# Kernel optimization log

Hardware: AMD Instinct MI355X
Metric: run time of the kernel (lower is better)

Reference implementation:

```python
import jax, jax.numpy as jnp
import numpy as np

N, DIM, H, D, S, B = 30000, 256, 8, 64, 32, 8
INNER = H * D


def setup_inputs() -> dict:
    key = jax.random.key(0)
    ks = jax.random.split(key, 16)
    def w(k, shape, fan_in):
        return jax.random.normal(k, shape, dtype=jnp.float32) / np.sqrt(fan_in)
    x = jax.random.normal(ks[0], (N, DIM), dtype=jnp.float32)
    batch = jnp.sort(jax.random.randint(ks[1], (N,), 0, B))
    return {
        'x': x,
        'batch': batch,
        'W_fx': w(ks[2], (DIM, INNER), DIM), 'b_fx': jnp.zeros((INNER,), jnp.float32),
        'W_x': w(ks[3], (DIM, INNER), DIM), 'b_x': jnp.zeros((INNER,), jnp.float32),
        'W_slice': w(ks[4], (D, S), D), 'b_slice': jnp.zeros((S,), jnp.float32),
        'graph_temp': 0.5 * jnp.ones((1, H, 1), jnp.float32),
        'W_q': w(ks[5], (D, D), D), 'W_k': w(ks[6], (D, D), D), 'W_v': w(ks[7], (D, D), D),
        'W_out': w(ks[8], (INNER, DIM), INNER), 'b_out': jnp.zeros((DIM,), jnp.float32),
    }


def reference(x, batch, W_fx, b_fx, W_x, b_x, W_slice, b_slice, graph_temp,
              W_q, W_k, W_v, W_out, b_out):
    n = x.shape[0]
    scale = D ** -0.5
    fx = (x @ W_fx + b_fx).reshape(n, H, D)   # [N,H,D]
    xm = (x @ W_x + b_x).reshape(n, H, D)     # [N,H,D]
    # per-node slice assignment weights, tempered softmax over slices
    logits = (jnp.einsum('nhd,ds->nhs', xm, W_slice) + b_slice) / graph_temp
    w = jax.nn.softmax(logits, axis=-1)       # [N,H,S]
    onehot = jax.nn.one_hot(batch, B, dtype=x.dtype)  # [N,B]
    # scatter-add pooling per graph: slice_norm[b,h,s], slice_token[b,h,s,d]
    slice_norm = jax.ops.segment_sum(w, batch, num_segments=B)  # [B,H,S]
    wb = w[:, None, :, :] * onehot[:, :, None, None]            # [N,B,H,S]
    slice_token = jnp.einsum('nbhs,nhd->bhsd', wb, fx)
    slice_token = slice_token / (slice_norm[..., None] + 1e-5)
    # small attention over slice tokens
    q = jnp.einsum('bhsd,de->bhse', slice_token, W_q)
    k = jnp.einsum('bhsd,de->bhse', slice_token, W_k)
    v = jnp.einsum('bhsd,de->bhse', slice_token, W_v)
    attn = jax.nn.softmax(jnp.einsum('bhsd,bhtd->bhst', q, k) * scale, axis=-1)
    out_tok = jnp.einsum('bhst,bhtd->bhsd', attn, v)            # [B,H,S,D]
    # gather back to nodes with weighted reduction over slices
    tmp = jnp.einsum('nhs,bhsd->nbhd', w, out_tok)              # [N,B,H,D]
    out_x = jnp.einsum('nb,nbhd->nhd', onehot, tmp).reshape(n, INNER)
    return out_x @ W_out + b_out
```

## Files before the change

kernel.cpp:

```cpp
#include <hip/hip_runtime.h>

#define NDIM 256
#define INNER 512
#define NH 8
#define ND 64
#define NS 32
#define NB 8
#define NP 30208

typedef __attribute__((ext_vector_type(8))) short short8;
typedef __attribute__((ext_vector_type(4))) float f32x4;

static __device__ __forceinline__ short f2bf(float f) {
  unsigned u = __float_as_uint(f);
  unsigned r = (u + 0x7fffu + ((u >> 16) & 1u)) >> 16;
  return (short)r;
}
static __device__ __forceinline__ float bf2f(short s) {
  return __uint_as_float(((unsigned)(unsigned short)s) << 16);
}

static __device__ __forceinline__ void gl_lds16(const void* g, void* l) {
  __builtin_amdgcn_global_load_lds(
      (const __attribute__((address_space(1))) unsigned int*)g,
      (__attribute__((address_space(3))) unsigned int*)l, 16, 0, 0);
}

__global__ __launch_bounds__(256) void k_xsplit(
    const float* __restrict__ x, short* __restrict__ Xh, short* __restrict__ Xl,
    int total4)
{
  int id = blockIdx.x * 256 + threadIdx.x;
  if (id >= total4) return;
  float4 v = *(const float4*)&x[(size_t)id * 4];
  short h0 = f2bf(v.x), h1 = f2bf(v.y), h2 = f2bf(v.z), h3 = f2bf(v.w);
  short4 hv = make_short4(h0, h1, h2, h3);
  short4 lv = make_short4(f2bf(v.x - bf2f(h0)), f2bf(v.y - bf2f(h1)),
                          f2bf(v.z - bf2f(h2)), f2bf(v.w - bf2f(h3)));
  *(short4*)&Xh[(size_t)id * 4] = hv;
  *(short4*)&Xl[(size_t)id * 4] = lv;
}

__global__ __launch_bounds__(256) void k_prep(
    const float* __restrict__ Wfx, const float* __restrict__ Wx,
    const float* __restrict__ bx, const float* __restrict__ Wsl,
    const float* __restrict__ bsl,
    short* __restrict__ Bt1h, short* __restrict__ Bt1l,
    float* __restrict__ bcomb, int* __restrict__ seg)
{
  int id = blockIdx.x * 256 + threadIdx.x;
  if (id < 131072) {
    int k = id >> 9, n = id & 511;
    float v = Wfx[k * 512 + n];
    short hi = f2bf(v); short lo = f2bf(v - bf2f(hi));
    Bt1h[n * 256 + k] = hi; Bt1l[n * 256 + k] = lo;
  } else if (id < 196608) {
    int e = id - 131072;
    int c = e & 255, k = e >> 8;
    int h = c >> 5, s = c & 31;
    float acc = 0.f;
    #pragma unroll 8
    for (int d = 0; d < 64; d++) acc += Wx[k * 512 + h * 64 + d] * Wsl[d * 32 + s];
    short hi = f2bf(acc); short lo = f2bf(acc - bf2f(hi));
    Bt1h[(512 + c) * 256 + k] = hi; Bt1l[(512 + c) * 256 + k] = lo;
  } else if (id < 196864) {
    int c = id - 196608;
    int h = c >> 5, s = c & 31;
    float acc = bsl[s];
    #pragma unroll 8
    for (int d = 0; d < 64; d++) acc += bx[h * 64 + d] * Wsl[d * 32 + s];
    bcomb[c] = acc;
  } else if (id < 196880) {
    int v = id - 196864;
    seg[v] = (v == 0) ? 0 : 0x7fffffff;
  }
}

__global__ __launch_bounds__(256) void k_segs(
    const int* __restrict__ batch, int* __restrict__ seg, int N)
{
  int i = blockIdx.x * 256 + threadIdx.x;
  if (i >= N) return;
  int b = batch[i];
  int p = (i == 0) ? -1 : batch[i - 1];
  for (int v = p + 1; v <= b; v++)
    if (v >= 1) atomicMin(&seg[v], i);
  if (i == N - 1)
    for (int v = b + 1; v <= 8; v++) atomicMin(&seg[v], N);
}

__global__ __launch_bounds__(512, 4) void k_fxw(
    const short* __restrict__ Xh, const short* __restrict__ Xl,
    const short* __restrict__ Bt1h, const short* __restrict__ Bt1l,
    const float* __restrict__ bfx, const float* __restrict__ bcomb,
    const float* __restrict__ gtemp,
    short* __restrict__ fxTh, short* __restrict__ fxTl,
    short* __restrict__ wh_out, short* __restrict__ wl_out,
    int N, int ntiles)
{
  __shared__ __align__(16) short smem[17408];
  short* AhL = &smem[0];
  short* AlL = &smem[4096];
  short* BhL = &smem[8192];
  short* BlL = &smem[12288];

  const int lid = blockIdx.x;
  const int xcd = lid & 7;
  const int idx = lid >> 3;
  const int ct  = idx % 6;
  const int rowt = xcd + 8 * (idx / 6);
  if (rowt >= ntiles) return;
  const int row0 = rowt * 128;
  const int tid = threadIdx.x;
  const int lane = tid & 63, l15 = lane & 15, quad = lane >> 4;
  const int wvi = tid >> 6;
  const int wm = wvi & 1, wn = wvi >> 1;
  const int ctbase = ct * 128;
  const int srow = lane & 15, schunk = lane >> 4;

  f32x4 acc[4][2];
  #pragma unroll
  for (int i = 0; i < 4; i++)
    #pragma unroll
    for (int j = 0; j < 2; j++) acc[i][j] = (f32x4){0.f, 0.f, 0.f, 0.f};

  for (int kt = 0; kt < 8; kt++) {
    {
      int gr = row0 + wvi * 16 + srow;
      if (gr > N - 1) gr = N - 1;
      size_t aoff = (size_t)gr * 256 + kt * 32 + schunk * 8;
      int br = ctbase + wvi * 16 + srow;
      size_t boff = (size_t)br * 256 + kt * 32 + schunk * 8;
      gl_lds16(Xh + aoff, AhL + wvi * 512);
      gl_lds16(Xl + aoff, AlL + wvi * 512);
      gl_lds16(Bt1h + boff, BhL + wvi * 512);
      gl_lds16(Bt1l + boff, BlL + wvi * 512);
    }
    __syncthreads();

    short8 ah[4], al[4];
    #pragma unroll
    for (int mt = 0; mt < 4; mt++) {
      int rg = wm * 4 + mt;
      ah[mt] = *(const short8*)&AhL[rg * 512 + quad * 128 + l15 * 8];
      al[mt] = *(const short8*)&AlL[rg * 512 + quad * 128 + l15 * 8];
    }
    #pragma unroll
    for (int nt = 0; nt < 2; nt++) {
      int rg = wn * 2 + nt;
      short8 bh = *(const short8*)&BhL[rg * 512 + quad * 128 + l15 * 8];
      short8 bl = *(const short8*)&BlL[rg * 512 + quad * 128 + l15 * 8];
      #pragma unroll
      for (int mt = 0; mt < 4; mt++) {
        acc[mt][nt] = __builtin_amdgcn_mfma_f32_16x16x32_bf16(ah[mt], bh, acc[mt][nt], 0, 0, 0);
        acc[mt][nt] = __builtin_amdgcn_mfma_f32_16x16x32_bf16(ah[mt], bl, acc[mt][nt], 0, 0, 0);
        acc[mt][nt] = __builtin_amdgcn_mfma_f32_16x16x32_bf16(al[mt], bh, acc[mt][nt], 0, 0, 0);
      }
    }
    __syncthreads();
  }

  if (ct < 4) {
    short (*T)[136] = (short(*)[136])&smem[0];
    #pragma unroll
    for (int pass = 0; pass < 2; pass++) {
      __syncthreads();
      #pragma unroll
      for (int nt = 0; nt < 2; nt++) {
        int cl = wn * 32 + nt * 16 + l15;
        float bias = bfx[ctbase + cl];
        #pragma unroll
        for (int mt = 0; mt < 4; mt++)
          #pragma unroll
          for (int r = 0; r < 4; r++) {
            int rl = wm * 64 + mt * 16 + quad * 4 + r;
            float v = acc[mt][nt][r] + bias;
            short hi2 = f2bf(v);
            T[cl][rl] = pass ? f2bf(v - bf2f(hi2)) : hi2;
          }
      }
      __syncthreads();
      short* dst = pass ? fxTl : fxTh;
      #pragma unroll
      for (int t = 0; t < 4; t++) {
        int idx2 = tid + t * 512;
        int row = idx2 >> 4, kc = (idx2 & 15) * 8;
        *(int4*)&dst[(size_t)(ctbase + row) * NP + row0 + kc] = *(const int4*)&T[row][kc];
      }
    }
  } else {
    int ct2 = ct - 4;
    int lcbase = ct2 * 128 + wn * 32;
    int h = lcbase >> 5;
    float inv_t = 1.0f / gtemp[h];
    int lc0 = lcbase + l15, lc1 = lcbase + 16 + l15;
    float b0 = bcomb[lc0], b1 = bcomb[lc1];
    #pragma unroll
    for (int mt = 0; mt < 4; mt++) {
      #pragma unroll
      for (int r = 0; r < 4; r++) {
        float s0 = (acc[mt][0][r] + b0) * inv_t;
        float s1 = (acc[mt][1][r] + b1) * inv_t;
        float m = fmaxf(s0, s1);
        #pragma unroll
        for (int off = 1; off < 16; off <<= 1) m = fmaxf(m, __shfl_xor(m, off, 16));
        float e0 = __expf(s0 - m), e1 = __expf(s1 - m);
        float sum = e0 + e1;
        #pragma unroll
        for (int off = 1; off < 16; off <<= 1) sum += __shfl_xor(sum, off, 16);
        float inv = 1.0f / sum;
        int row = row0 + wm * 64 + mt * 16 + quad * 4 + r;
        if (row < N) {
          float w0v = e0 * inv, w1v = e1 * inv;
          size_t base = (size_t)row * (NH * NS);
          short h0 = f2bf(w0v), h1 = f2bf(w1v);
          wh_out[base + lc0] = h0; wl_out[base + lc0] = f2bf(w0v - bf2f(h0));
          wh_out[base + lc1] = h1; wl_out[base + lc1] = f2bf(w1v - bf2f(h1));
        }
      }
    }
  }
}

__global__ __launch_bounds__(256) void k_scat(
    const short* __restrict__ wh, const short* __restrict__ wl,
    const short* __restrict__ fxTh, const short* __restrict__ fxTl,
    const int* __restrict__ seg,
    float* __restrict__ stok, float* __restrict__ snorm, int N)
{
  __shared__ short wth[32][136];
  __shared__ short wtl[32][136];
  __shared__ short fh[64][136];
  __shared__ short fl[64][136];
  __shared__ float ln[32];

  const int h = blockIdx.y;
  const int n0 = blockIdx.x * 512;
  const int tid = threadIdx.x;
  const int lane = tid & 63, l15 = lane & 15, quad = lane >> 4;
  const int wv = tid >> 6;
  const int nend = min(n0 + 512, N);

  f32x4 acc0 = (f32x4){0.f, 0.f, 0.f, 0.f};
  f32x4 acc1 = (f32x4){0.f, 0.f, 0.f, 0.f};

  for (int b = 0; b < NB; b++) {
    int lo = max(seg[b], n0), hi = min(seg[b + 1], nend);
    if (lo >= hi) continue;
    if (tid < 32) ln[tid] = 0.f;
    int c0lo = (lo - n0) & ~127;
    int c0hi = hi - n0;
    for (int c0 = c0lo; c0 < c0hi; c0 += 128) {
      __syncthreads();
      #pragma unroll
      for (int t = 0; t < 2; t++) {
        int idx2 = tid + t * 256;
        int row = idx2 >> 2;
        int sc  = (idx2 & 3) * 8;
        int ng = n0 + c0 + row;
        short8 vh = (short8){0,0,0,0,0,0,0,0};
        short8 vl = (short8){0,0,0,0,0,0,0,0};
        if (ng >= lo && ng < hi) {
          size_t src = (size_t)ng * 256 + h * 32 + sc;
          vh = *(const short8*)&wh[src];
          vl = *(const short8*)&wl[src];
        }
        #pragma unroll
        for (int j = 0; j < 8; j++) {
          wth[sc + j][row] = vh[j];
          wtl[sc + j][row] = vl[j];
        }
      }
      #pragma unroll
      for (int t = 0; t < 4; t++) {
        int idx2 = tid + t * 256;
        int row = idx2 >> 4, kc = (idx2 & 15) * 8;
        size_t src = (size_t)(h * 64 + row) * NP + n0 + c0 + kc;
        *(int4*)&fh[row][kc] = *(const int4*)&fxTh[src];
        *(int4*)&fl[row][kc] = *(const int4*)&fxTl[src];
      }
      __syncthreads();

      {
        int s = tid >> 3, g = tid & 7;
        float sum = 0.f;
        #pragma unroll
        for (int i2 = 0; i2 < 16; i2++) {
          int nl = g * 16 + i2;
          sum += bf2f(wth[s][nl]) + bf2f(wtl[s][nl]);
        }
        atomicAdd(&ln[s], sum);
      }

      for (int k0 = 0; k0 < 128; k0 += 32) {
        int gbase = n0 + c0 + k0;
        if (gbase + 32 <= lo || gbase >= hi) continue;
        short8 a0h = *(const short8*)&wth[l15][k0 + quad * 8];
        short8 a0l = *(const short8*)&wtl[l15][k0 + quad * 8];
        short8 a1h = *(const short8*)&wth[16 + l15][k0 + quad * 8];
        short8 a1l = *(const short8*)&wtl[16 + l15][k0 + quad * 8];
        short8 bh = *(const short8*)&fh[wv * 16 + l15][k0 + quad * 8];
        short8 bl = *(const short8*)&fl[wv * 16 + l15][k0 + quad * 8];
        acc0 = __builtin_amdgcn_mfma_f32_16x16x32_bf16(a0h, bh, acc0, 0, 0, 0);
        acc0 = __builtin_amdgcn_mfma_f32_16x16x32_bf16(a0h, bl, acc0, 0, 0, 0);
        acc0 = __builtin_amdgcn_mfma_f32_16x16x32_bf16(a0l, bh, acc0, 0, 0, 0);
        acc1 = __builtin_amdgcn_mfma_f32_16x16x32_bf16(a1h, bh, acc1, 0, 0, 0);
        acc1 = __builtin_amdgcn_mfma_f32_16x16x32_bf16(a1h, bl, acc1, 0, 0, 0);
        acc1 = __builtin_amdgcn_mfma_f32_16x16x32_bf16(a1l, bh, acc1, 0, 0, 0);
      }
    }
    __syncthreads();
    size_t base = ((size_t)b * NH + h) * NS;
    #pragma unroll
    for (int r = 0; r < 4; r++) {
      atomicAdd(&stok[(base + quad * 4 + r) * ND + wv * 16 + l15], acc0[r]);
      atomicAdd(&stok[(base + 16 + quad * 4 + r) * ND + wv * 16 + l15], acc1[r]);
    }
    if (tid < 32) atomicAdd(&snorm[base + tid], ln[tid]);
    acc0 = (f32x4){0.f, 0.f, 0.f, 0.f};
    acc1 = (f32x4){0.f, 0.f, 0.f, 0.f};
    __syncthreads();
  }
}

__global__ __launch_bounds__(256) void k_attn(
    const float* __restrict__ stok, const float* __restrict__ snorm,
    const float* __restrict__ Wq, const float* __restrict__ Wk,
    const float* __restrict__ Wv, const float* __restrict__ Wout,
    short* __restrict__ PTh, short* __restrict__ PTl)
{
  __shared__ float st[32][65];
  __shared__ float qs[32][65];
  __shared__ float ks[32][65];
  __shared__ float vs[32][65];
  __shared__ float at[32][33];
  __shared__ float ot[32][65];
  const int bh = blockIdx.x;
  const int b = bh >> 3, h = bh & 7;
  const int tid = threadIdx.x;

  for (int i = tid; i < 2048; i += 256) {
    int ss = i >> 6;
    float nrm = snorm[(size_t)bh * NS + ss] + 1e-5f;
    st[ss][i & 63] = stok[(size_t)bh * 2048 + i] / nrm;
  }
  __syncthreads();

  const int e = tid & 63, sgp = tid >> 6;
  for (int ii = 0; ii < 8; ii++) {
    int ss = sgp * 8 + ii;
    float aq = 0.f, ak = 0.f, av = 0.f;
    #pragma unroll 8
    for (int dd = 0; dd < 64; dd++) {
      float sv = st[ss][dd];
      aq += sv * Wq[dd * 64 + e];
      ak += sv * Wk[dd * 64 + e];
      av += sv * Wv[dd * 64 + e];
    }
    qs[ss][e] = aq; ks[ss][e] = ak; vs[ss][e] = av;
  }
  __syncthreads();

  const float scale = 0.125f;
  for (int i = tid; i < 1024; i += 256) {
    int si = i >> 5, tj = i & 31;
    float a = 0.f;
    #pragma unroll 8
    for (int ee = 0; ee < 64; ee++) a += qs[si][ee] * ks[tj][ee];
    at[si][tj] = a * scale;
  }
  __syncthreads();

  if (tid < 32) {
    float m = -1e30f;
    for (int j = 0; j < 32; j++) m = fmaxf(m, at[tid][j]);
    float sum = 0.f;
    for (int j = 0; j < 32; j++) { float ev = __expf(at[tid][j] - m); at[tid][j] = ev; sum += ev; }
    float inv = 1.f / sum;
    for (int j = 0; j < 32; j++) at[tid][j] *= inv;
  }
  __syncthreads();

  for (int ii = 0; ii < 8; ii++) {
    int ss = sgp * 8 + ii;
    float a = 0.f;
    #pragma unroll 8
    for (int tj = 0; tj < 32; tj++) a += at[ss][tj] * vs[tj][e];
    ot[ss][e] = a;
  }
  __syncthreads();

  const int s_p = tid >> 3;
  const int c0 = (tid & 7) * 32;
  float pacc[32];
  #pragma unroll
  for (int q = 0; q < 32; q++) pacc[q] = 0.f;
  for (int dd = 0; dd < 64; dd++) {
    float o = ot[s_p][dd];
    const float4* wr = (const float4*)&Wout[(size_t)(h * 64 + dd) * NDIM + c0];
    #pragma unroll
    for (int q = 0; q < 8; q++) {
      float4 v = wr[q];
      pacc[4 * q + 0] += o * v.x;
      pacc[4 * q + 1] += o * v.y;
      pacc[4 * q + 2] += o * v.z;
      pacc[4 * q + 3] += o * v.w;
    }
  }
  #pragma unroll
  for (int q = 0; q < 32; q++) {
    int c = c0 + q;
    float val = pacc[q];
    short hi = f2bf(val);
    size_t dst = ((size_t)b * NDIM + c) * 256 + h * 32 + s_p;
    PTh[dst] = hi;
    PTl[dst] = f2bf(val - bf2f(hi));
  }
}

__global__ __launch_bounds__(256) void k_outw(
    const short* __restrict__ wh, const short* __restrict__ wl,
    const short* __restrict__ PTh, const short* __restrict__ PTl,
    const int* __restrict__ batch, const float* __restrict__ bout,
    float* __restrict__ out, int N)
{
  __shared__ short Ah[128][40];
  __shared__ short Al[128][40];
  __shared__ short Bh[128][40];
  __shared__ short Bl[128][40];
  __shared__ int b_sh[128];

  const int ct = blockIdx.x;
  const int row0 = blockIdx.y * 128;
  const int tid = threadIdx.x;
  const int lane = tid & 63, l15 = lane & 15, quad = lane >> 4;
  const int wv = tid >> 6, wm = wv & 1, wn = wv >> 1;
  const int ctbase = ct * 128;
  const int cnt = min(128, N - row0);

  if (tid < 128) b_sh[tid] = (tid < cnt) ? batch[row0 + tid] : -1;
  __syncthreads();

  f32x4 acc[4][4];
  #pragma unroll
  for (int i = 0; i < 4; i++)
    #pragma unroll
    for (int j = 0; j < 4; j++) acc[i][j] = (f32x4){0.f, 0.f, 0.f, 0.f};

  int i0 = 0;
  while (i0 < cnt) {
    int b = b_sh[i0];
    int j = i0;
    while (j < cnt && b_sh[j] == b) j++;

    for (int kt = 0; kt < 8; kt++) {
      #pragma unroll
      for (int t = 0; t < 2; t++) {
        int i = tid + t * 256;
        int row = i >> 2, kc = (i & 3) * 8;
        int4 vh = make_int4(0, 0, 0, 0), vl = make_int4(0, 0, 0, 0);
        if (row >= i0 && row < j) {
          size_t src = (size_t)(row0 + row) * 256 + kt * 32 + kc;
          vh = *(const int4*)&wh[src];
          vl = *(const int4*)&wl[src];
        }
        *(int4*)&Ah[row][kc] = vh;
        *(int4*)&Al[row][kc] = vl;
      }
      #pragma unroll
      for (int t = 0; t < 2; t++) {
        int i = tid + t * 256;
        int row = i >> 2, kc = (i & 3) * 8;
        size_t src = ((size_t)b * NDIM + ctbase + row) * 256 + kt * 32 + kc;
        *(int4*)&Bh[row][kc] = *(const int4*)&PTh[src];
        *(int4*)&Bl[row][kc] = *(const int4*)&PTl[src];
      }
      __syncthreads();

      short8 ah[4], al[4];
      #pragma unroll
      for (int mt = 0; mt < 4; mt++) {
        int m = wm * 64 + mt * 16 + l15;
        ah[mt] = *(const short8*)&Ah[m][quad * 8];
        al[mt] = *(const short8*)&Al[m][quad * 8];
      }
      #pragma unroll
      for (int nt = 0; nt < 4; nt++) {
        int n = wn * 64 + nt * 16 + l15;
        short8 bh = *(const short8*)&Bh[n][quad * 8];
        short8 bl = *(const short8*)&Bl[n][quad * 8];
        #pragma unroll
        for (int mt = 0; mt < 4; mt++) {
          acc[mt][nt] = __builtin_amdgcn_mfma_f32_16x16x32_bf16(ah[mt], bh, acc[mt][nt], 0, 0, 0);
          acc[mt][nt] = __builtin_amdgcn_mfma_f32_16x16x32_bf16(ah[mt], bl, acc[mt][nt], 0, 0, 0);
          acc[mt][nt] = __builtin_amdgcn_mfma_f32_16x16x32_bf16(al[mt], bh, acc[mt][nt], 0, 0, 0);
        }
      }
      __syncthreads();
    }
    i0 = j;
  }

  #pragma unroll
  for (int nt = 0; nt < 4; nt++) {
    int c = ctbase + wn * 64 + nt * 16 + l15;
    float bias = bout[c];
    #pragma unroll
    for (int mt = 0; mt < 4; mt++)
      #pragma unroll
      for (int r = 0; r < 4; r++) {
        int row = row0 + wm * 64 + mt * 16 + quad * 4 + r;
        if (row < N) out[(size_t)row * NDIM + c] = acc[mt][nt][r] + bias;
      }
  }
}

extern "C" void kernel_launch(void* const* d_in, const int* in_sizes, int n_in,
                              void* d_out, int out_size, void* d_ws, size_t ws_size,
                              hipStream_t stream) {
  const float* x      = (const float*)d_in[0];
  const int*   batch  = (const int*)d_in[1];
  const float* Wfx    = (const float*)d_in[2];
  const float* bfx    = (const float*)d_in[3];
  const float* Wx     = (const float*)d_in[4];
  const float* bx     = (const float*)d_in[5];
  const float* Wsl    = (const float*)d_in[6];
  const float* bsl    = (const float*)d_in[7];
  const float* gtemp  = (const float*)d_in[8];
  const float* Wq     = (const float*)d_in[9];
  const float* Wk     = (const float*)d_in[10];
  const float* Wv     = (const float*)d_in[11];
  const float* Wout   = (const float*)d_in[12];
  const float* bout   = (const float*)d_in[13];
  float* out = (float*)d_out;

  const int N = in_sizes[0] / NDIM;

  float* stok  = (float*)d_ws;
  float* snorm = stok + 131072;
  float* bcomb = snorm + 2048;
  int*   seg   = (int*)(bcomb + 256);
  short* Bt1h  = (short*)(seg + 16);
  short* Bt1l  = Bt1h + 196608;
  short* Xh    = Bt1l + 196608;
  short* Xl    = Xh + 7680000;
  short* whb   = Xl + 7680000;
  short* wlb   = whb + (size_t)NP * 256;
  short* fxTh  = wlb + (size_t)NP * 256;
  short* fxTl  = fxTh + (size_t)512 * NP;
  short* PTh   = fxTl + (size_t)512 * NP;
  short* PTl   = PTh + 524288;

  hipMemsetAsync(stok, 0, (size_t)(131072 + 2048) * sizeof(float), stream);

  k_xsplit<<<(N * 64 + 255) / 256, 256, 0, stream>>>(x, Xh, Xl, N * 64);

  k_prep<<<770, 256, 0, stream>>>(Wfx, Wx, bx, Wsl, bsl, Bt1h, Bt1l, bcomb, seg);

  k_segs<<<(N + 255) / 256, 256, 0, stream>>>(batch, seg, N);

  const int ntiles = (N + 127) / 128;
  const int qmax = (ntiles + 7) / 8;
  k_fxw<<<8 * qmax * 6, 512, 0, stream>>>(Xh, Xl, Bt1h, Bt1l, bfx, bcomb, gtemp,
                                          fxTh, fxTl, whb, wlb, N, ntiles);

  dim3 g2((N + 511) / 512, NH);
  k_scat<<<g2, 256, 0, stream>>>(whb, wlb, fxTh, fxTl, seg, stok, snorm, N);

  k_attn<<<NB * NH, 256, 0, stream>>>(stok, snorm, Wq, Wk, Wv, Wout, PTh, PTl);

  dim3 g5(2, (N + 127) / 128);
  k_outw<<<g5, 256, 0, stream>>>(whb, wlb, PTh, PTl, batch, bout, out, N);
}
```

Measured before the change: 329.3 us.

## Register-tile attention kernel, stage Wout in LDS, vectorize bf16 split stores

Result: faster. 269.7 us (-18.1%).

```diff
diff --git a/kernel.cpp b/kernel.cpp
--- a/kernel.cpp
+++ b/kernel.cpp
@@ -329,92 +329,173 @@
     const float* __restrict__ Wv, const float* __restrict__ Wout,
     short* __restrict__ PTh, short* __restrict__ PTl)
 {
-  __shared__ float st[32][65];
-  __shared__ float qs[32][65];
-  __shared__ float ks[32][65];
-  __shared__ float vs[32][65];
-  __shared__ float at[32][33];
-  __shared__ float ot[32][65];
+  __shared__ __align__(16) float st[32][68];
+  __shared__ __align__(16) float qs[32][68];
+  __shared__ __align__(16) float ks[32][68];
+  __shared__ __align__(16) float vs[32][68];
+  __shared__ __align__(16) float at[32][36];
+  __shared__ __align__(16) float ot[32][68];
+  __shared__ __align__(16) float wo[64][256];
+
   const int bh = blockIdx.x;
   const int b = bh >> 3, h = bh & 7;
   const int tid = threadIdx.x;
+  const int lane = tid & 63;
+  const int wv = tid >> 6;
+
+  {
+    const float* wsrc = Wout + (size_t)h * 16384;
+    float* wdst = &wo[0][0];
+    #pragma unroll
+    for (int r = 0; r < 16; r++) {
+      int off = r * 1024 + wv * 256;
+      gl_lds16(wsrc + off + lane * 4, wdst + off);
+    }
+  }
 
   for (int i = tid; i < 2048; i += 256) {
-    int ss = i >> 6;
+    int ss = i >> 6, dd = i & 63;
     float nrm = snorm[(size_t)bh * NS + ss] + 1e-5f;
-    st[ss][i & 63] = stok[(size_t)bh * 2048 + i] / nrm;
+    st[ss][dd] = stok[(size_t)bh * 2048 + i] / nrm;
   }
   __syncthreads();
 
-  const int e = tid & 63, sgp = tid >> 6;
-  for (int ii = 0; ii < 8; ii++) {
-    int ss = sgp * 8 + ii;
-    float aq = 0.f, ak = 0.f, av = 0.f;
-    #pragma unroll 8
-    for (int dd = 0; dd < 64; dd++) {
-      float sv = st[ss][dd];
-      aq += sv * Wq[dd * 64 + e];
-      ak += sv * Wk[dd * 64 + e];
-      av += sv * Wv[dd * 64 + e];
-    }
-    qs[ss][e] = aq; ks[ss][e] = ak; vs[ss][e] = av;
+  {
+    float aq[8], ak[8], av[8];
+    #pragma unroll
+    for (int i = 0; i < 8; i++) { aq[i] = 0.f; ak[i] = 0.f; av[i] = 0.f; }
+    for (int ch = 0; ch < 16; ch++) {
+      float4 sv[8];
+      #pragma unroll
+      for (int i = 0; i < 8; i++) sv[i] = *(const float4*)&st[wv * 8 + i][ch * 4];
+      #pragma unroll
+      for (int d = 0; d < 4; d++) {
+        int dd = ch * 4 + d;
+        float wq = Wq[dd * 64 + lane];
+        float wk = Wk[dd * 64 + lane];
+        float wvv = Wv[dd * 64 + lane];
+        #pragma unroll
+        for (int i = 0; i < 8; i++) {
+          float sd = (d == 0) ? sv[i].x : (d == 1) ? sv[i].y : (d == 2) ? sv[i].z : sv[i].w;
+          aq[i] = fmaf(sd, wq, aq[i]);
+          ak[i] = fmaf(sd, wk, ak[i]);
+          av[i] = fmaf(sd, wvv, av[i]);
+        }
+      }
+    }
+    #pragma unroll
+    for (int i = 0; i < 8; i++) {
+      qs[wv * 8 + i][lane] = aq[i];
+      ks[wv * 8 + i][lane] = ak[i];
+      vs[wv * 8 + i][lane] = av[i];
+    }
   }
   __syncthreads();
 
-  const float scale = 0.125f;
-  for (int i = tid; i < 1024; i += 256) {
-    int si = i >> 5, tj = i & 31;
-    float a = 0.f;
-    #pragma unroll 8
-    for (int ee = 0; ee < 64; ee++) a += qs[si][ee] * ks[tj][ee];
-    at[si][tj] = a * scale;
+  {
+    const int si = tid >> 3, tj0 = (tid & 7) * 4;
+    float a0 = 0.f, a1 = 0.f, a2 = 0.f, a3 = 0.f;
+    for (int ch = 0; ch < 16; ch++) {
+      float4 q4 = *(const float4*)&qs[si][ch * 4];
+      float4 k0 = *(const float4*)&ks[tj0 + 0][ch * 4];
+      float4 k1 = *(const float4*)&ks[tj0 + 1][ch * 4];
+      float4 k2 = *(const float4*)&ks[tj0 + 2][ch * 4];
+      float4 k3 = *(const float4*)&ks[tj0 + 3][ch * 4];
+      a0 += q4.x * k0.x + q4.y * k0.y + q4.z * k0.z + q4.w * k0.w;
+      a1 += q4.x * k1.x + q4.y * k1.y + q4.z * k1.z + q4.w * k1.w;
+      a2 += q4.x * k2.x + q4.y * k2.y + q4.z * k2.z + q4.w * k2.w;
+      a3 += q4.x * k3.x + q4.y * k3.y + q4.z * k3.z + q4.w * k3.w;
+    }
+    const float scale = 0.125f;
+    *(float4*)&at[si][tj0] = (float4){a0 * scale, a1 * scale, a2 * scale, a3 * scale};
   }
   __syncthreads();
 
-  if (tid < 32) {
-    float m = -1e30f;
-    for (int j = 0; j < 32; j++) m = fmaxf(m, at[tid][j]);
-    float sum = 0.f;
-    for (int j = 0; j < 32; j++) { float ev = __expf(at[tid][j] - m); at[tid][j] = ev; sum += ev; }
-    float inv = 1.f / sum;
-    for (int j = 0; j < 32; j++) at[tid][j] *= inv;
+  {
+    const int row = tid >> 3, jb = (tid & 7) * 4;
+    float4 v = *(const float4*)&at[row][jb];
+    float m = fmaxf(fmaxf(v.x, v.y), fmaxf(v.z, v.w));
+    #pragma unroll
+    for (int off = 1; off < 8; off <<= 1) m = fmaxf(m, __shfl_xor(m, off, 8));
+    float e0 = __expf(v.x - m), e1 = __expf(v.y - m);
+    float e2 = __expf(v.z - m), e3 = __expf(v.w - m);
+    float s = e0 + e1 + e2 + e3;
+    #pragma unroll
+    for (int off = 1; off < 8; off <<= 1) s += __shfl_xor(s, off, 8);
+    float inv = 1.f / s;
+    *(float4*)&at[row][jb] = (float4){e0 * inv, e1 * inv, e2 * inv, e3 * inv};
   }
   __syncthreads();
 
-  for (int ii = 0; ii < 8; ii++) {
-    int ss = sgp * 8 + ii;
-    float a = 0.f;
-    #pragma unroll 8
-    for (int tj = 0; tj < 32; tj++) a += at[ss][tj] * vs[tj][e];
-    ot[ss][e] = a;
+  {
+    float acc[8];
+    #pragma unroll
+    for (int i = 0; i < 8; i++) acc[i] = 0.f;
+    for (int ch = 0; ch < 8; ch++) {
+      float v0 = vs[ch * 4 + 0][lane];
+      float v1 = vs[ch * 4 + 1][lane];
+      float v2 = vs[ch * 4 + 2][lane];
+      float v3 = vs[ch * 4 + 3][lane];
+      #pragma unroll
+      for (int i = 0; i < 8; i++) {
+        float4 a4 = *(const float4*)&at[wv * 8 + i][ch * 4];
+        acc[i] += a4.x * v0 + a4.y * v1 + a4.z * v2 + a4.w * v3;
+      }
+    }
+    #pragma unroll
+    for (int i = 0; i < 8; i++) ot[wv * 8 + i][lane] = acc[i];
   }
   __syncthreads();
 
-  const int s_p = tid >> 3;
-  const int c0 = (tid & 7) * 32;
-  float pacc[32];
-  #pragma unroll
-  for (int q = 0; q < 32; q++) pacc[q] = 0.f;
-  for (int dd = 0; dd < 64; dd++) {
-    float o = ot[s_p][dd];
-    const float4* wr = (const float4*)&Wout[(size_t)(h * 64 + dd) * NDIM + c0];
-    #pragma unroll
-    for (int q = 0; q < 8; q++) {
-      float4 v = wr[q];
-      pacc[4 * q + 0] += o * v.x;
-      pacc[4 * q + 1] += o * v.y;
-      pacc[4 * q + 2] += o * v.z;
-      pacc[4 * q + 3] += o * v.w;
-    }
-  }
-  #pragma unroll
-  for (int q = 0; q < 32; q++) {
-    int c = c0 + q;
-    float val = pacc[q];
-    short hi = f2bf(val);
-    size_t dst = ((size_t)b * NDIM + c) * 256 + h * 32 + s_p;
-    PTh[dst] = hi;
-    PTl[dst] = f2bf(val - bf2f(hi));
+  {
+    const int c0 = 4 * (lane & 31) + 128 * (lane >> 5);
+    float pacc[8][4];
+    #pragma unroll
+    for (int i = 0; i < 8; i++)
+      #pragma unroll
+      for (int c = 0; c < 4; c++) pacc[i][c] = 0.f;
+
+    for (int ch = 0; ch < 16; ch++) {
+      float4 w0 = *(const float4*)&wo[ch * 4 + 0][c0];
+      float4 w1 = *(const float4*)&wo[ch * 4 + 1][c0];
+      float4 w2 = *(const float4*)&wo[ch * 4 + 2][c0];
+      float4 w3 = *(const float4*)&wo[ch * 4 + 3][c0];
+      #pragma unroll
+      for (int i = 0; i < 8; i++) {
+        float4 o4 = *(const float4*)&ot[wv * 8 + i][ch * 4];
+        pacc[i][0] = fmaf(o4.x, w0.x, pacc[i][0]);
+        pacc[i][1] = fmaf(o4.x, w0.y, pacc[i][1]);
+        pacc[i][2] = fmaf(o4.x, w0.z, pacc[i][2]);
+        pacc[i][3] = fmaf(o4.x, w0.w, pacc[i][3]);
+        pacc[i][0] = fmaf(o4.y, w1.x, pacc[i][0]);
+        pacc[i][1] = fmaf(o4.y, w1.y, pacc[i][1]);
+        pacc[i][2] = fmaf(o4.y, w1.z, pacc[i][2]);
+        pacc[i][3] = fmaf(o4.y, w1.w, pacc[i][3]);
+        pacc[i][0] = fmaf(o4.z, w2.x, pacc[i][0]);
+        pacc[i][1] = fmaf(o4.z, w2.y, pacc[i][1]);
+        pacc[i][2] = fmaf(o4.z, w2.z, pacc[i][2]);
+        pacc[i][3] = fmaf(o4.z, w2.w, pacc[i][3]);
+        pacc[i][0] = fmaf(o4.w, w3.x, pacc[i][0]);
+        pacc[i][1] = fmaf(o4.w, w3.y, pacc[i][1]);
+        pacc[i][2] = fmaf(o4.w, w3.z, pacc[i][2]);
+        pacc[i][3] = fmaf(o4.w, w3.w, pacc[i][3]);
+      }
+    }
+
+    #pragma unroll
+    for (int cc = 0; cc < 4; cc++) {
+      short8 hv, lv;
+      #pragma unroll
+      for (int i = 0; i < 8; i++) {
+        float val = pacc[i][cc];
+        short hi = f2bf(val);
+        hv[i] = hi;
+        lv[i] = f2bf(val - bf2f(hi));
+      }
+      size_t dst = ((size_t)b * NDIM + (c0 + cc)) * 256 + h * 32 + wv * 8;
+      *(short8*)&PTh[dst] = hv;
+      *(short8*)&PTl[dst] = lv;
+    }
   }
 }
 
```
